# Kernel tuning notes

Hardware: AMD Instinct MI355X
Metric: run time of the kernel (lower is better)

## Reference

```python
import jax, jax.numpy as jnp
import numpy as np

N, L, E, H = 4, 2048, 512, 8
D = E // H


def setup_inputs() -> dict:
    key = jax.random.key(0)
    ks = jax.random.split(key, 8)
    causal = jnp.tril(jnp.ones((L, L), dtype=bool))[None, None]  # [1,1,L,L]
    return {
        "values": jax.random.normal(ks[0], (N, L, E), dtype=jnp.float32),
        "keys": jax.random.normal(ks[1], (N, L, E), dtype=jnp.float32),
        "query": jax.random.normal(ks[2], (N, L, E), dtype=jnp.float32),
        "mask": causal,
        "Wv": jax.random.normal(ks[3], (D, D), dtype=jnp.float32) * 0.05,
        "Wk": jax.random.normal(ks[4], (D, D), dtype=jnp.float32) * 0.05,
        "Wq": jax.random.normal(ks[5], (D, D), dtype=jnp.float32) * 0.05,
        "Wo": jax.random.normal(ks[6], (E, E), dtype=jnp.float32) * 0.05,
        "bo": jnp.zeros((E,), dtype=jnp.float32),
    }


def reference(values, keys, query, mask, Wv, Wk, Wq, Wo, bo):
    n, ql, e = query.shape
    # split heads: [N, len, H, D]
    v = values.reshape(n, -1, H, D)
    k = keys.reshape(n, -1, H, D)
    q = query.reshape(n, ql, H, D)
    # per-head linear projections (nn.Linear: x @ W.T, no bias)
    v = jnp.einsum("nlhd,od->nlho", v, Wv)
    k = jnp.einsum("nlhd,od->nlho", k, Wk)
    q = jnp.einsum("nqhd,od->nqho", q, Wq)
    # scores [N, H, Q, K]
    energy = jnp.einsum("nqhd,nkhd->nhqk", q, k)
    energy = jnp.where(mask == 0, jnp.float32(-1e28), energy)
    # NOTE: module scales by embed_size**0.5, not head_dim**0.5 (faithful)
    attn = jax.nn.softmax(energy / np.float32(e ** 0.5), axis=3)
    out = jnp.einsum("nhqk,nkhd->nqhd", attn, v).reshape(n, ql, e)
    return out @ Wo.T + bo
```

## Files before the change

kernel.cpp:

```cpp
#include <hip/hip_runtime.h>

#define NB 4
#define LL 2048
#define EE 512
#define HH 8
#define DD 64

typedef __attribute__((ext_vector_type(8))) short short8;
typedef __attribute__((ext_vector_type(4))) float f32x4;
typedef __attribute__((ext_vector_type(16))) float f32x16;
typedef __attribute__((ext_vector_type(4))) unsigned int u32x4;
typedef __attribute__((ext_vector_type(2))) int i32x2;
typedef __bf16 bf16x8 __attribute__((ext_vector_type(8)));

#if __has_builtin(__builtin_amdgcn_exp2f)
#define EXP2(x) __builtin_amdgcn_exp2f(x)
#else
#define EXP2(x) __expf((x) * 0.6931471805599453f)
#endif

#define QSCALE (0.04419417382415922f * 1.4426950408889634f)
#define MSHIFT 4.0f

static __device__ __forceinline__ short bfc(float f) {
    return __builtin_bit_cast(short, (__bf16)f);
}

static __device__ __forceinline__ unsigned pkbf(float lo, float hi) {
    unsigned short a = (unsigned short)(unsigned)__builtin_bit_cast(unsigned short, (__bf16)lo);
    unsigned short b = (unsigned short)(unsigned)__builtin_bit_cast(unsigned short, (__bf16)hi);
    return (unsigned)a | ((unsigned)b << 16);
}

static __device__ __forceinline__ f32x4 mfma16(short8 a, short8 b, f32x4 c) {
    return __builtin_amdgcn_mfma_f32_16x16x32_bf16(
        __builtin_bit_cast(bf16x8, a), __builtin_bit_cast(bf16x8, b), c, 0, 0, 0);
}

static __device__ __forceinline__ f32x16 mfma32(short8 a, short8 b, f32x16 c) {
    return __builtin_amdgcn_mfma_f32_32x32x16_bf16(
        __builtin_bit_cast(bf16x8, a), __builtin_bit_cast(bf16x8, b), c, 0, 0, 0);
}

__global__ __launch_bounds__(256, 4) void k_proj(const float* __restrict__ vals,
                                                 const float* __restrict__ keys,
                                                 const float* __restrict__ qry,
                                                 const float* __restrict__ Wv,
                                                 const float* __restrict__ Wk,
                                                 const float* __restrict__ Wq,
                                                 const float* __restrict__ Wo,
                                                 unsigned short* __restrict__ Qp,
                                                 unsigned short* __restrict__ Kp,
                                                 unsigned short* __restrict__ Vg,
                                                 unsigned short* __restrict__ Wob) {
    __shared__ __align__(16) unsigned short smem[20480];

    const int tid = threadIdx.x;
    const int w = tid >> 6, ln = tid & 63;
    const int c = ln & 15, g = ln >> 4;

    if (blockIdx.x < 512) {
        unsigned short (*kq)[8256] = (unsigned short (*)[8256])smem;
        const int r0 = blockIdx.x * 128;
        const int n = r0 >> 14;
        const int l0 = (r0 >> 3) & (LL - 1);
        const int h = c & 7;

#pragma unroll
        for (int t = 0; t < 2; ++t) {
            const float* X = t ? qry : keys;
            const float* W = t ? Wq : Wk;

            short8 xf[2][2];
#pragma unroll
            for (int rt = 0; rt < 2; ++rt) {
                const int r = r0 + w * 32 + rt * 16 + c;
#pragma unroll
                for (int kk = 0; kk < 2; ++kk) {
                    const float* p = X + (size_t)r * DD + kk * 32 + g * 8;
                    short8 v;
#pragma unroll
                    for (int j = 0; j < 8; ++j) v[j] = bfc(p[j]);
                    xf[rt][kk] = v;
                }
            }
            short8 wf[4][2];
#pragma unroll
            for (int nt = 0; nt < 4; ++nt)
#pragma unroll
                for (int kk = 0; kk < 2; ++kk) {
                    const float* p = W + (nt * 16 + c) * DD + kk * 32 + g * 8;
                    short8 v;
#pragma unroll
                    for (int j = 0; j < 8; ++j) v[j] = bfc(p[j]);
                    wf[nt][kk] = v;
                }

#pragma unroll
            for (int rt = 0; rt < 2; ++rt) {
                const int l15 = w * 4 + rt * 2 + (c >> 3);
#pragma unroll
                for (int nt = 0; nt < 4; ++nt) {
                    f32x4 acc = {0.f, 0.f, 0.f, 0.f};
                    acc = mfma16(wf[nt][0], xf[rt][0], acc);
                    acc = mfma16(wf[nt][1], xf[rt][1], acc);
                    const int o = nt * 16 + g * 4;
                    const float s = t ? QSCALE : 1.0f;
                    uint2 u = {pkbf(acc[0] * s, acc[1] * s), pkbf(acc[2] * s, acc[3] * s)};
                    *(uint2*)&kq[t][h * 1032 + l15 * 64 + o] = u;
                }
            }
        }
        __syncthreads();

#pragma unroll
        for (int t = 0; t < 2; ++t) {
            unsigned short* dstb = t ? Qp : Kp;
            const int hh = tid >> 5, s = tid & 31;
#pragma unroll
            for (int i = 0; i < 4; ++i) {
                const int q = s * 4 + i;
                const int l = q >> 3, cc = q & 7;
                uint4 v = *(const uint4*)&kq[t][hh * 1032 + l * 64 + cc * 8];
                *(uint4*)(dstb + ((size_t)(n * HH + hh) * LL + l0 + l) * DD + cc * 8) = v;
            }
        }
    } else {
        {
            const int i = (blockIdx.x - 512) * 1024 + tid * 4;
            float4 v = *(const float4*)(Wo + i);
            Wob[i + 0] = (unsigned short)bfc(v.x);
            Wob[i + 1] = (unsigned short)bfc(v.y);
            Wob[i + 2] = (unsigned short)bfc(v.z);
            Wob[i + 3] = (unsigned short)bfc(v.w);
        }
        unsigned short* vv = smem;
        const int r0 = (blockIdx.x - 512) * 256;
        const int n = r0 >> 14;
        const int l0 = (r0 >> 3) & (LL - 1);
        const int h = c & 7;

        short8 wf[4][2];
#pragma unroll
        for (int nt = 0; nt < 4; ++nt)
#pragma unroll
            for (int kk = 0; kk < 2; ++kk) {
                const float* p = Wv + (nt * 16 + c) * DD + kk * 32 + g * 8;
                short8 v;
#pragma unroll
                for (int j = 0; j < 8; ++j) v[j] = bfc(p[j]);
                wf[nt][kk] = v;
            }

#pragma unroll
        for (int rg = 0; rg < 2; ++rg) {
            short8 xf[2][2];
#pragma unroll
            for (int rt = 0; rt < 2; ++rt) {
                const int r = r0 + rg * 128 + w * 32 + rt * 16 + c;
#pragma unroll
                for (int kk = 0; kk < 2; ++kk) {
                    const float* p = vals + (size_t)r * DD + kk * 32 + g * 8;
                    short8 v;
#pragma unroll
                    for (int j = 0; j < 8; ++j) v[j] = bfc(p[j]);
                    xf[rt][kk] = v;
                }
            }
#pragma unroll
            for (int rt = 0; rt < 2; ++rt) {
                const int l31 = rg * 16 + w * 4 + rt * 2 + (c >> 3);
#pragma unroll
                for (int nt = 0; nt < 4; ++nt) {
                    f32x4 acc = {0.f, 0.f, 0.f, 0.f};
                    acc = mfma16(wf[nt][0], xf[rt][0], acc);
                    acc = mfma16(wf[nt][1], xf[rt][1], acc);
                    const int o = nt * 16 + g * 4;
#pragma unroll
                    for (int reg = 0; reg < 4; ++reg)
                        vv[h * 2560 + (o + reg) * 40 + l31] = (unsigned short)bfc(acc[reg]);
                }
            }
        }
        __syncthreads();

#pragma unroll
        for (int pi = 0; pi < 2; ++pi) {
            const int p = tid + pi * 256;
            const int hh = p >> 6, d = p & 63;
            const unsigned short* sp = &vv[hh * 2560 + d * 40];
            uint4 c0a = *(const uint4*)(sp + 0);
            uint4 c0b = *(const uint4*)(sp + 8);
            uint4 c1a = *(const uint4*)(sp + 16);
            uint4 c1b = *(const uint4*)(sp + 24);
            unsigned short* dst = Vg + (size_t)(n * HH + hh) * (LL * DD) +
                                  (size_t)(l0 >> 4) * 1024 + d * 16;
            *(uint4*)(dst + 0) = c0a;
            *(uint4*)(dst + 8) = c0b;
            *(uint4*)(dst + 1024) = c1a;
            *(uint4*)(dst + 1032) = c1b;
        }
    }
}

static __device__ __forceinline__ void stage_tile(const unsigned short* __restrict__ src,
                                                  unsigned short* buf, int w, int ln,
                                                  size_t rstride) {
#pragma unroll
    for (int r = 0; r < 2; ++r) {
        int qi = w * 2 + r;
        int row = qi * 8 + (ln >> 3);
        int s = (ln & 7) ^ (row & 7);
        __builtin_amdgcn_global_load_lds(
            (const __attribute__((address_space(1))) unsigned int*)(src + (size_t)row * rstride + s * 8),
            (__attribute__((address_space(3))) unsigned int*)(buf + qi * 512),
            16, 0, 0);
    }
}

static __device__ __forceinline__ void stage_v(const unsigned short* __restrict__ src,
                                               unsigned short* buf, int w, int ln) {
#pragma unroll
    for (int r = 0; r < 2; ++r) {
        int idx = w * 64 + ln + r * 256;
        int d = idx >> 3, c16 = idx & 7;
        int cc = c16 ^ (d & 7);
        __builtin_amdgcn_global_load_lds(
            (const __attribute__((address_space(1))) unsigned int*)(src + (cc >> 1) * 1024 + d * 16 + (cc & 1) * 8),
            (__attribute__((address_space(3))) unsigned int*)(buf + idx * 8),
            16, 0, 0);
    }
}

__global__ __launch_bounds__(256, 4) void k_attn(const unsigned short* __restrict__ Qp,
                                                 const unsigned short* __restrict__ Kp,
                                                 const unsigned short* __restrict__ Vg,
                                                 unsigned short* __restrict__ Xa) {
    __shared__ __align__(16) unsigned short Kt[2][64 * 64];
    __shared__ __align__(16) unsigned short Vt[2][64 * 64];

    const int tid = threadIdx.x;
    const int w = tid >> 6, ln = tid & 63;
    const int c31 = ln & 31, g2 = ln >> 5;
    const int qpair = w >> 1, kvh = w & 1;

    const int b = blockIdx.x;
    const int x8 = b & 7;
    const int idx = b >> 3;
    const int nh = (x8 << 2) | (idx & 3);
    const int jj = (idx >> 2) & 15;
    const int j = (idx >> 6) ? jj : 31 - jj;
    const int qt = 2 * j + qpair;
    const int Q0 = qt * 32;
    const int nIter = j + 1;

    const unsigned short* Qb = Qp + (size_t)nh * (LL * DD);
    const unsigned short* Kb = Kp + (size_t)nh * (LL * DD);
    const unsigned short* Vb = Vg + (size_t)nh * (LL * DD);

    short8 qf[4];
#pragma unroll
    for (int kc = 0; kc < 4; ++kc)
        qf[kc] = *(const short8*)(Qb + (Q0 + c31) * DD + kc * 16 + g2 * 8);

    f32x16 oacc0, oacc1;
#pragma unroll
    for (int r = 0; r < 16; ++r) { oacc0[r] = 0.f; oacc1[r] = 0.f; }
    float lsum = 0.f;

    stage_tile(Kb, &Kt[0][0], w, ln, DD);
    stage_v(Vb, &Vt[0][0], w, ln);
    __syncthreads();

    int cur = 0;
    for (int t = 0; t < nIter; ++t) {
        const int nxt = cur ^ 1;
        if (t + 1 < nIter) {
            stage_tile(Kb + (size_t)(t + 1) * (64 * DD), &Kt[nxt][0], w, ln, DD);
            stage_v(Vb + (size_t)(t + 1) * 4096, &Vt[nxt][0], w, ln);
        }

        const int kb32 = t * 64 + kvh * 32;
        if (kb32 <= Q0 + 31) {
            const char* kb_ = (const char*)&Kt[cur][0];
            const char* vb_ = (const char*)&Vt[cur][0];
            const int q = Q0 + c31;

            f32x16 sc;
#pragma unroll
            for (int r = 0; r < 16; ++r) sc[r] = -MSHIFT;
            {
                const int R = kvh * 32 + c31;
                const unsigned rb = (unsigned)(R * 128);
                const unsigned swz = (unsigned)((R & 7) << 4);
#pragma unroll
                for (int kc = 0; kc < 4; ++kc) {
                    short8 af = *(const short8*)(kb_ + rb + (((unsigned)(kc * 32 + g2 * 16)) ^ swz));
                    sc = mfma32(af, qf[kc], sc);
                }
            }

            if (kb32 + 31 > Q0) {
#pragma unroll
                for (int r = 0; r < 16; ++r) {
                    int kvg = kb32 + (r & 3) + 8 * (r >> 2) + 4 * g2;
                    sc[r] = (kvg > q) ? -1e30f : sc[r];
                }
            }

#pragma unroll
            for (int r = 0; r < 16; ++r) sc[r] = EXP2(sc[r]);
            {
                float a[8];
#pragma unroll
                for (int r = 0; r < 8; ++r) a[r] = sc[r] + sc[r + 8];
                float b0 = a[0] + a[4], b1 = a[1] + a[5];
                float b2 = a[2] + a[6], b3 = a[3] + a[7];
                lsum += (b0 + b1) + (b2 + b3);
            }

            unsigned pk[8];
#pragma unroll
            for (int iw = 0; iw < 8; ++iw) pk[iw] = pkbf(sc[2 * iw], sc[2 * iw + 1]);
#pragma unroll
            for (int ck = 0; ck < 2; ++ck) {
                unsigned s0 = g2 ? pk[4 * ck + 0] : pk[4 * ck + 2];
                unsigned s1 = g2 ? pk[4 * ck + 1] : pk[4 * ck + 3];
                unsigned x0 = __shfl_xor(s0, 32);
                unsigned x1 = __shfl_xor(s1, 32);
                u32x4 bfv;
                bfv[0] = g2 ? x0 : pk[4 * ck + 0];
                bfv[1] = g2 ? x1 : pk[4 * ck + 1];
                bfv[2] = g2 ? pk[4 * ck + 2] : x0;
                bfv[3] = g2 ? pk[4 * ck + 3] : x1;
                short8 pB = __builtin_bit_cast(short8, bfv);
                const unsigned coff = (unsigned)(kvh * 64 + ck * 32 + g2 * 16);
                {
                    const int dP = c31;
                    short8 A = *(const short8*)(vb_ + (unsigned)(dP * 128) +
                                                (coff ^ ((unsigned)((dP & 7) << 4))));
                    oacc0 = mfma32(A, pB, oacc0);
                }
                {
                    const int dP = 32 + c31;
                    short8 A = *(const short8*)(vb_ + (unsigned)(dP * 128) +
                                                (coff ^ ((unsigned)((dP & 7) << 4))));
                    oacc1 = mfma32(A, pB, oacc1);
                }
            }
        }

        __syncthreads();
        cur = nxt;
    }

    {
        float* lb = (float*)(&Kt[0][0]);
        float* ob = (float*)(&Vt[0][0]);
        if (kvh) {
            float* op = ob + qpair * 2048;
#pragma unroll
            for (int r = 0; r < 16; ++r) {
                op[r * 64 + ln] = oacc0[r];
                op[(16 + r) * 64 + ln] = oacc1[r];
            }
            lb[qpair * 64 + ln] = lsum;
        }
        __syncthreads();
        if (kvh) return;
        {
            const float* op = ob + qpair * 2048;
#pragma unroll
            for (int r = 0; r < 16; ++r) {
                oacc0[r] += op[r * 64 + ln];
                oacc1[r] += op[(16 + r) * 64 + ln];
            }
            lsum += lb[qpair * 64 + ln];
        }
    }

    lsum += __shfl_xor(lsum, 32);
    const float inv = 1.0f / lsum;
    const int n = nh >> 3, h = nh & 7;
    unsigned short* orow = Xa + ((size_t)(n * LL + Q0 + c31)) * EE + h * DD;
#pragma unroll
    for (int a = 0; a < 4; ++a) {
        {
            float e0 = oacc0[4 * a + 0] * inv, e1 = oacc0[4 * a + 1] * inv;
            float e2 = oacc0[4 * a + 2] * inv, e3 = oacc0[4 * a + 3] * inv;
            uint2 u = {pkbf(e0, e1), pkbf(e2, e3)};
            *(uint2*)(orow + a * 8 + g2 * 4) = u;
        }
        {
            float e0 = oacc1[4 * a + 0] * inv, e1 = oacc1[4 * a + 1] * inv;
            float e2 = oacc1[4 * a + 2] * inv, e3 = oacc1[4 * a + 3] * inv;
            uint2 u = {pkbf(e0, e1), pkbf(e2, e3)};
            *(uint2*)(orow + 32 + a * 8 + g2 * 4) = u;
        }
    }
}

__global__ __launch_bounds__(256) void k_out(const unsigned short* __restrict__ X,
                                             const unsigned short* __restrict__ Wob,
                                             const float* __restrict__ bo,
                                             float* __restrict__ out) {
    const int tid = threadIdx.x, w = tid >> 6, ln = tid & 63, c = ln & 15, g = ln >> 4;
    const int b = blockIdx.x;
    const int x8 = b & 7, jj = b >> 3;
    const int mb = x8 * 8 + (jj & 7);
    const int nb = jj >> 3;
    const int mbase = mb * 128 + w * 16;
    const int nbase = nb * 64;

    const unsigned short* Xr0 = X + (size_t)(mbase + c) * EE + g * 8;
    const unsigned short* Xr1 = X + (size_t)(mbase + 64 + c) * EE + g * 8;
    const unsigned short* Wr = Wob + (size_t)(nbase + c) * EE + g * 8;

    f32x4 acc0[4] = {}, acc1[4] = {};
    short8 a0 = *(const short8*)(Xr0);
    short8 a1 = *(const short8*)(Xr1);
    short8 bf[4];
#pragma unroll
    for (int nt = 0; nt < 4; ++nt) bf[nt] = *(const short8*)(Wr + (size_t)nt * 16 * EE);

#pragma unroll
    for (int ks = 0; ks < 16; ++ks) {
        short8 na0, na1, nbf[4];
        if (ks < 15) {
            na0 = *(const short8*)(Xr0 + (ks + 1) * 32);
            na1 = *(const short8*)(Xr1 + (ks + 1) * 32);
#pragma unroll
            for (int nt = 0; nt < 4; ++nt)
                nbf[nt] = *(const short8*)(Wr + (size_t)nt * 16 * EE + (ks + 1) * 32);
        }
#pragma unroll
        for (int nt = 0; nt < 4; ++nt) {
            acc0[nt] = mfma16(a0, bf[nt], acc0[nt]);
            acc1[nt] = mfma16(a1, bf[nt], acc1[nt]);
        }
        if (ks < 15) {
            a0 = na0; a1 = na1;
#pragma unroll
            for (int nt = 0; nt < 4; ++nt) bf[nt] = nbf[nt];
        }
    }
#pragma unroll
    for (int nt = 0; nt < 4; ++nt) {
        float bias = bo[nbase + nt * 16 + c];
#pragma unroll
        for (int reg = 0; reg < 4; ++reg) {
            int row0 = mbase + g * 4 + reg;
            out[(size_t)row0 * EE + nbase + nt * 16 + c] = acc0[nt][reg] + bias;
            out[(size_t)(row0 + 64) * EE + nbase + nt * 16 + c] = acc1[nt][reg] + bias;
        }
    }
}

extern "C" void kernel_launch(void* const* d_in, const int* in_sizes, int n_in,
                              void* d_out, int out_size, void* d_ws, size_t ws_size,
                              hipStream_t stream) {
    const float* vals = (const float*)d_in[0];
    const float* keys = (const float*)d_in[1];
    const float* qry  = (const float*)d_in[2];
    const float* Wv = (const float*)d_in[4];
    const float* Wk = (const float*)d_in[5];
    const float* Wq = (const float*)d_in[6];
    const float* Wo = (const float*)d_in[7];
    const float* bo = (const float*)d_in[8];
    float* out = (float*)d_out;

    char* ws = (char*)d_ws;
    unsigned short* Qp  = (unsigned short*)(ws);
    unsigned short* Kp  = (unsigned short*)(ws + (8u  << 20));
    unsigned short* Vg  = (unsigned short*)(ws + (16u << 20));
    unsigned short* Xa  = (unsigned short*)(ws + (24u << 20));
    unsigned short* Wob = (unsigned short*)(ws + (32u << 20));

    hipLaunchKernelGGL(k_proj, dim3(768), dim3(256), 0, stream,
                       vals, keys, qry, Wv, Wk, Wq, Wo, Qp, Kp, Vg, Wob);
    hipLaunchKernelGGL(k_attn, dim3(1024), dim3(256), 0, stream, Qp, Kp, Vg, Xa);
    hipLaunchKernelGGL(k_out, dim3(512), dim3(256), 0, stream, Xa, Wob, bo, out);
}
```

Baseline: 87.99 us.

## Widen attention KV tile to 128 keys per iteration, halving loop trips and barriers

Each iteration of the attention kernel now stages 128 keys of K and V instead of 64, and each KV-half wave pair handles two 32-key subtiles. This halves the number of loop iterations and __syncthreads barriers, and gives each wave more MFMA work between synchronisations. In exchange LDS use doubles to 64 KB per block and launch bounds drop to 2 blocks per CU. That lowers occupancy, and for small j the causal skip wastes more of each tile.

```diff
diff --git a/kernel.cpp b/kernel.cpp
--- a/kernel.cpp
+++ b/kernel.cpp
@@ -203,27 +203,27 @@
     }
 }
 
-static __device__ __forceinline__ void stage_tile(const unsigned short* __restrict__ src,
-                                                  unsigned short* buf, int w, int ln,
+static __device__ __forceinline__ void stage_k128(const unsigned short* __restrict__ src,
+                                                  unsigned short* buf, int tid,
                                                   size_t rstride) {
 #pragma unroll
-    for (int r = 0; r < 2; ++r) {
-        int qi = w * 2 + r;
-        int row = qi * 8 + (ln >> 3);
-        int s = (ln & 7) ^ (row & 7);
+    for (int r = 0; r < 4; ++r) {
+        int idx = r * 256 + tid;
+        int row = idx >> 3;
+        int s = (idx & 7) ^ (row & 7);
         __builtin_amdgcn_global_load_lds(
             (const __attribute__((address_space(1))) unsigned int*)(src + (size_t)row * rstride + s * 8),
-            (__attribute__((address_space(3))) unsigned int*)(buf + qi * 512),
+            (__attribute__((address_space(3))) unsigned int*)(buf + idx * 8),
             16, 0, 0);
     }
 }
 
-static __device__ __forceinline__ void stage_v(const unsigned short* __restrict__ src,
-                                               unsigned short* buf, int w, int ln) {
-#pragma unroll
-    for (int r = 0; r < 2; ++r) {
-        int idx = w * 64 + ln + r * 256;
-        int d = idx >> 3, c16 = idx & 7;
+static __device__ __forceinline__ void stage_v128(const unsigned short* __restrict__ src,
+                                                  unsigned short* buf, int tid) {
+#pragma unroll
+    for (int r = 0; r < 4; ++r) {
+        int idx = r * 256 + tid;
+        int d = idx >> 4, c16 = idx & 15;
         int cc = c16 ^ (d & 7);
         __builtin_amdgcn_global_load_lds(
             (const __attribute__((address_space(1))) unsigned int*)(src + (cc >> 1) * 1024 + d * 16 + (cc & 1) * 8),
@@ -232,12 +232,12 @@
     }
 }
 
-__global__ __launch_bounds__(256, 4) void k_attn(const unsigned short* __restrict__ Qp,
+__global__ __launch_bounds__(256, 2) void k_attn(const unsigned short* __restrict__ Qp,
                                                  const unsigned short* __restrict__ Kp,
                                                  const unsigned short* __restrict__ Vg,
                                                  unsigned short* __restrict__ Xa) {
-    __shared__ __align__(16) unsigned short Kt[2][64 * 64];
-    __shared__ __align__(16) unsigned short Vt[2][64 * 64];
+    __shared__ __align__(16) unsigned short Kt[2][128 * 64];
+    __shared__ __align__(16) unsigned short Vt[2][64 * 128];
 
     const int tid = threadIdx.x;
     const int w = tid >> 6, ln = tid & 63;
@@ -252,7 +252,7 @@
     const int j = (idx >> 6) ? jj : 31 - jj;
     const int qt = 2 * j + qpair;
     const int Q0 = qt * 32;
-    const int nIter = j + 1;
+    const int nIter = (j + 2) >> 1;
 
     const unsigned short* Qb = Qp + (size_t)nh * (LL * DD);
     const unsigned short* Kb = Kp + (size_t)nh * (LL * DD);
@@ -268,84 +268,87 @@
     for (int r = 0; r < 16; ++r) { oacc0[r] = 0.f; oacc1[r] = 0.f; }
     float lsum = 0.f;
 
-    stage_tile(Kb, &Kt[0][0], w, ln, DD);
-    stage_v(Vb, &Vt[0][0], w, ln);
+    stage_k128(Kb, &Kt[0][0], tid, DD);
+    stage_v128(Vb, &Vt[0][0], tid);
     __syncthreads();
 
     int cur = 0;
     for (int t = 0; t < nIter; ++t) {
         const int nxt = cur ^ 1;
         if (t + 1 < nIter) {
-            stage_tile(Kb + (size_t)(t + 1) * (64 * DD), &Kt[nxt][0], w, ln, DD);
-            stage_v(Vb + (size_t)(t + 1) * 4096, &Vt[nxt][0], w, ln);
-        }
-
-        const int kb32 = t * 64 + kvh * 32;
-        if (kb32 <= Q0 + 31) {
-            const char* kb_ = (const char*)&Kt[cur][0];
-            const char* vb_ = (const char*)&Vt[cur][0];
-            const int q = Q0 + c31;
-
-            f32x16 sc;
-#pragma unroll
-            for (int r = 0; r < 16; ++r) sc[r] = -MSHIFT;
-            {
-                const int R = kvh * 32 + c31;
-                const unsigned rb = (unsigned)(R * 128);
-                const unsigned swz = (unsigned)((R & 7) << 4);
-#pragma unroll
-                for (int kc = 0; kc < 4; ++kc) {
-                    short8 af = *(const short8*)(kb_ + rb + (((unsigned)(kc * 32 + g2 * 16)) ^ swz));
-                    sc = mfma32(af, qf[kc], sc);
-                }
-            }
-
-            if (kb32 + 31 > Q0) {
-#pragma unroll
-                for (int r = 0; r < 16; ++r) {
-                    int kvg = kb32 + (r & 3) + 8 * (r >> 2) + 4 * g2;
-                    sc[r] = (kvg > q) ? -1e30f : sc[r];
-                }
-            }
-
-#pragma unroll
-            for (int r = 0; r < 16; ++r) sc[r] = EXP2(sc[r]);
-            {
-                float a[8];
-#pragma unroll
-                for (int r = 0; r < 8; ++r) a[r] = sc[r] + sc[r + 8];
-                float b0 = a[0] + a[4], b1 = a[1] + a[5];
-                float b2 = a[2] + a[6], b3 = a[3] + a[7];
-                lsum += (b0 + b1) + (b2 + b3);
-            }
-
-            unsigned pk[8];
-#pragma unroll
-            for (int iw = 0; iw < 8; ++iw) pk[iw] = pkbf(sc[2 * iw], sc[2 * iw + 1]);
-#pragma unroll
-            for (int ck = 0; ck < 2; ++ck) {
-                unsigned s0 = g2 ? pk[4 * ck + 0] : pk[4 * ck + 2];
-                unsigned s1 = g2 ? pk[4 * ck + 1] : pk[4 * ck + 3];
-                unsigned x0 = __shfl_xor(s0, 32);
-                unsigned x1 = __shfl_xor(s1, 32);
-                u32x4 bfv;
-                bfv[0] = g2 ? x0 : pk[4 * ck + 0];
-                bfv[1] = g2 ? x1 : pk[4 * ck + 1];
-                bfv[2] = g2 ? pk[4 * ck + 2] : x0;
-                bfv[3] = g2 ? pk[4 * ck + 3] : x1;
-                short8 pB = __builtin_bit_cast(short8, bfv);
-                const unsigned coff = (unsigned)(kvh * 64 + ck * 32 + g2 * 16);
+            stage_k128(Kb + (size_t)(t + 1) * (128 * DD), &Kt[nxt][0], tid, DD);
+            stage_v128(Vb + (size_t)(t + 1) * 8192, &Vt[nxt][0], tid);
+        }
+
+        const char* kb_ = (const char*)&Kt[cur][0];
+        const char* vb_ = (const char*)&Vt[cur][0];
+        const int q = Q0 + c31;
+
+#pragma unroll
+        for (int st = 0; st < 2; ++st) {
+            const int kb32 = t * 128 + kvh * 64 + st * 32;
+            if (kb32 <= Q0 + 31) {
+                f32x16 sc;
+#pragma unroll
+                for (int r = 0; r < 16; ++r) sc[r] = -MSHIFT;
                 {
-                    const int dP = c31;
-                    short8 A = *(const short8*)(vb_ + (unsigned)(dP * 128) +
-                                                (coff ^ ((unsigned)((dP & 7) << 4))));
-                    oacc0 = mfma32(A, pB, oacc0);
-                }
+                    const int R = kvh * 64 + st * 32 + c31;
+                    const unsigned rb = (unsigned)(R * 128);
+                    const unsigned swz = (unsigned)((R & 7) << 4);
+#pragma unroll
+                    for (int kc = 0; kc < 4; ++kc) {
+                        short8 af = *(const short8*)(kb_ + rb + (((unsigned)(kc * 32 + g2 * 16)) ^ swz));
+                        sc = mfma32(af, qf[kc], sc);
+                    }
+                }
+
+                if (kb32 + 31 > Q0) {
+#pragma unroll
+                    for (int r = 0; r < 16; ++r) {
+                        int kvg = kb32 + (r & 3) + 8 * (r >> 2) + 4 * g2;
+                        sc[r] = (kvg > q) ? -1e30f : sc[r];
+                    }
+                }
+
+#pragma unroll
+                for (int r = 0; r < 16; ++r) sc[r] = EXP2(sc[r]);
                 {
-                    const int dP = 32 + c31;
-                    short8 A = *(const short8*)(vb_ + (unsigned)(dP * 128) +
-                                                (coff ^ ((unsigned)((dP & 7) << 4))));
-                    oacc1 = mfma32(A, pB, oacc1);
+                    float a[8];
+#pragma unroll
+                    for (int r = 0; r < 8; ++r) a[r] = sc[r] + sc[r + 8];
+                    float b0 = a[0] + a[4], b1 = a[1] + a[5];
+                    float b2 = a[2] + a[6], b3 = a[3] + a[7];
+                    lsum += (b0 + b1) + (b2 + b3);
+                }
+
+                unsigned pk[8];
+#pragma unroll
+                for (int iw = 0; iw < 8; ++iw) pk[iw] = pkbf(sc[2 * iw], sc[2 * iw + 1]);
+#pragma unroll
+                for (int ck = 0; ck < 2; ++ck) {
+                    unsigned s0 = g2 ? pk[4 * ck + 0] : pk[4 * ck + 2];
+                    unsigned s1 = g2 ? pk[4 * ck + 1] : pk[4 * ck + 3];
+                    unsigned x0 = __shfl_xor(s0, 32);
+                    unsigned x1 = __shfl_xor(s1, 32);
+                    u32x4 bfv;
+                    bfv[0] = g2 ? x0 : pk[4 * ck + 0];
+                    bfv[1] = g2 ? x1 : pk[4 * ck + 1];
+                    bfv[2] = g2 ? pk[4 * ck + 2] : x0;
+                    bfv[3] = g2 ? pk[4 * ck + 3] : x1;
+                    short8 pB = __builtin_bit_cast(short8, bfv);
+                    const unsigned coff = (unsigned)(kvh * 128 + st * 64 + ck * 32 + g2 * 16);
+                    {
+                        const int dP = c31;
+                        short8 A = *(const short8*)(vb_ + (unsigned)(dP * 256) +
+                                                    (coff ^ ((unsigned)((dP & 7) << 4))));
+                        oacc0 = mfma32(A, pB, oacc0);
+                    }
+                    {
+                        const int dP = 32 + c31;
+                        short8 A = *(const short8*)(vb_ + (unsigned)(dP * 256) +
+                                                    (coff ^ ((unsigned)((dP & 7) << 4))));
+                        oacc1 = mfma32(A, pB, oacc1);
+                    }
                 }
             }
         }
```

Result: slower. 95.51 us (+8.5%).
